# Performance work log

Hardware: AMD Instinct MI355X
Metric: run time of the kernel (lower is better)

Reference implementation:

```python
import jax, jax.numpy as jnp
import numpy as np
from jax import lax

EMB, HDIM, OBS_LEN = 64, 64, 8
BATCH, NSCENES, SCENE = 32768, 4096, 8
SEQ_LEN = 12


def setup_inputs() -> dict:
    key = jax.random.key(0)
    ks = jax.random.split(key, 16)
    obs_traj = jax.random.normal(ks[0], (OBS_LEN, BATCH, 2), jnp.float32)
    last_pos = jax.random.normal(ks[1], (BATCH, 2), jnp.float32)
    last_pos_rel = jax.random.normal(ks[2], (BATCH, 2), jnp.float32)
    starts = jnp.arange(NSCENES, dtype=jnp.int32) * SCENE
    seq_start_end = jnp.stack([starts, starts + SCENE], axis=1)  # (NSCENES, 2)
    # spatial_embedding: Linear(2, EMB)
    W_se = jax.random.normal(ks[3], (EMB, 2), jnp.float32) * 0.5
    b_se = jax.random.normal(ks[4], (EMB,), jnp.float32) * 0.1
    # weight-normed convs: w = g * v / ||v||_(in,k) per out-channel, bias init zero
    def conv_params(k, cout, cin, ksz):
        ka, kb = jax.random.split(k)
        std = np.sqrt(4.0 / (ksz * cin))
        v = jax.random.normal(ka, (cout, cin, ksz), jnp.float32) * std
        g = jax.random.uniform(kb, (cout,), jnp.float32, 0.5, 1.5)
        b = jnp.zeros((cout,), jnp.float32)
        return v, g, b
    v1, g1, b1 = conv_params(ks[5], HDIM, EMB, 3)
    v2, g2, b2 = conv_params(ks[6], HDIM // 2, HDIM, 3)
    v3, g3, b3 = conv_params(ks[7], HDIM // 2, HDIM // 2, 3)
    # hidden2pos: Linear(2*HDIM, 2)
    W_hp = jax.random.normal(ks[8], (2, 2 * HDIM), jnp.float32) * 0.05
    b_hp = jax.random.normal(ks[9], (2,), jnp.float32) * 0.05
    return {"obs_traj": obs_traj, "last_pos": last_pos, "last_pos_rel": last_pos_rel,
            "W_se": W_se, "b_se": b_se,
            "v1": v1, "g1": g1, "b1": b1,
            "v2": v2, "g2": g2, "b2": b2,
            "v3": v3, "g3": g3, "b3": b3,
            "W_hp": W_hp, "b_hp": b_hp,
            "seq_start_end": seq_start_end, "seq_len": SEQ_LEN}


def _wn_conv_relu(x, v, g, b):
    # weight-norm: w[o] = g[o] * v[o] / ||v[o]||  (norm over in-channels and kernel)
    norm = jnp.sqrt(jnp.sum(v * v, axis=(1, 2)))
    w = v * (g / norm)[:, None, None]
    y = lax.conv_general_dilated(x, w, (1,), 'VALID',
                                 dimension_numbers=('NCH', 'OIH', 'NCH'))
    return jax.nn.relu(y + b[None, :, None])


def reference(obs_traj, last_pos, last_pos_rel,
              W_se, b_se, v1, g1, b1, v2, g2, b2, v3, g3, b3, W_hp, b_hp,
              seq_start_end, seq_len):
    batch = last_pos.shape[0]
    nseg = seq_start_end.shape[0]
    h_dim = v1.shape[0]
    # scene id for each pedestrian (segments are contiguous [start,end) ranges)
    seg = jnp.searchsorted(seq_start_end[:, 0], jnp.arange(batch), side='right') - 1
    # obs_traj embedding -> (batch, EMB, OBS_LEN)
    emb = obs_traj @ W_se.T + b_se            # (T, B, EMB)
    obs_emb0 = jnp.transpose(emb, (1, 2, 0))  # (B, EMB, T)

    def step(carry, _):
        obs_emb, lp = carry
        s = _wn_conv_relu(obs_emb, v1, g1, b1)   # (B, H, T-2)
        s = _wn_conv_relu(s, v2, g2, b2)         # (B, H/2, T-4)
        s = _wn_conv_relu(s, v3, g3, b3)         # (B, H/2, T-6)
        s = s.reshape(batch, h_dim)              # (H/2)*(T-6) == H
        mx = jax.ops.segment_max(s, seg, num_segments=nseg)  # ragged per-scene max
        st = jnp.concatenate([s, mx[seg]], axis=1)           # (B, 2H)
        rel = st @ W_hp.T + b_hp                 # (B, 2)
        lp = rel + lp
        dec = rel @ W_se.T + b_se                # (B, EMB)
        obs_emb = jnp.concatenate([obs_emb[:, :, 1:], dec[:, :, None]], axis=2)
        return (obs_emb, lp), rel

    _, rels = lax.scan(step, (obs_emb0, last_pos), None, length=seq_len)
    return rels  # (seq_len, batch, 2)
```

## Files before the change

kernel.cpp:

```cpp
#include <hip/hip_runtime.h>

#define BATCH 32768
#define SEQLEN 12
#define NBLK 512

typedef short short8 __attribute__((ext_vector_type(8)));
typedef float f32x4 __attribute__((ext_vector_type(4)));
typedef unsigned short ushort_t;

static __device__ __forceinline__ unsigned short f2bf(float x) {
    unsigned u = __float_as_uint(x);
    return (unsigned short)((u + 0x7FFFu + ((u >> 16) & 1u)) >> 16);
}
static __device__ __forceinline__ float bf2f(unsigned short h) {
    return __uint_as_float(((unsigned)h) << 16);
}

#define MFMA __builtin_amdgcn_mfma_f32_16x16x32_bf16


#define C1PED(PX, PY, QX, QY, RX, RY, PPED) do {                              \
    float v_ = cK1;                                                           \
    v_ = fmaf(ccA0, PX, v_); v_ = fmaf(ccB0, PY, v_);                         \
    v_ = fmaf(ccA1, QX, v_); v_ = fmaf(ccB1, QY, v_);                         \
    v_ = fmaf(ccA2, RX, v_); v_ = fmaf(ccB2, RY, v_);                         \
    v_ = fmaxf(v_, 0.f);                                                      \
    ushort_t h_ = f2bf(v_);                                                   \
    s1sh[wv][PPED][lane] = h_;                                                \
    s1sl[wv][PPED][lane] = f2bf(v_ - bf2f(h_));                               \
} while(0)

#define S1_FRAGREAD(SL) do {                                                  \
    s1fh[SL][0] = *(const short8*)&s1sh[wv][n][kg*8];                         \
    s1fh[SL][1] = *(const short8*)&s1sh[wv][n][32 + kg*8];                    \
    s1fl[SL][0] = *(const short8*)&s1sl[wv][n][kg*8];                         \
    s1fl[SL][1] = *(const short8*)&s1sl[wv][n][32 + kg*8];                    \
} while(0)

#define CONV1COL(SA, SB, SC, SL) do {                                         \
    _Pragma("unroll")                                                         \
    for (int pp_ = 0; pp_ < 8; ++pp_) {                                       \
        float4 fa_ = *(const float4*)&pos_s[wv][SA][2*pp_][0];                \
        float4 fb_ = *(const float4*)&pos_s[wv][SB][2*pp_][0];                \
        float4 fc_ = *(const float4*)&pos_s[wv][SC][2*pp_][0];                \
        C1PED(fa_.x, fa_.y, fb_.x, fb_.y, fc_.x, fc_.y, 2*pp_);               \
        C1PED(fa_.z, fa_.w, fb_.z, fb_.w, fc_.z, fc_.w, 2*pp_+1);             \
    }                                                                         \
    S1_FRAGREAD(SL);                                                          \
} while(0)

#define CONV2COL(CM3) do {                                                    \
    _Pragma("unroll")                                                         \
    for (int T = 0; T < 2; ++T) {                                             \
        f32x4 a1 = {0.f,0.f,0.f,0.f}, a2 = {0.f,0.f,0.f,0.f},                 \
              a3 = {0.f,0.f,0.f,0.f};                                         \
        _Pragma("unroll")                                                     \
        for (int kb = 0; kb < 6; ++kb) {                                      \
            const int sl = ((CM3) + (kb >> 1)) % 3, ich = kb & 1;             \
            const short8 wh = *(const short8*)&c2wh[T*6+kb][lane][0];         \
            const short8 wl = *(const short8*)&c2wl[T*6+kb][lane][0];         \
            a1 = MFMA(wh, s1fh[sl][ich], a1, 0, 0, 0);                        \
            a2 = MFMA(wh, s1fl[sl][ich], a2, 0, 0, 0);                        \
            a3 = MFMA(wl, s1fh[sl][ich], a3, 0, 0, 0);                        \
        }                                                                     \
        const float4 bb = *(const float4*)&b2s[T*16 + kg*4];                  \
        float w0 = fmaxf(a1[0]+a2[0]+a3[0]+bb.x, 0.f);                        \
        float w1 = fmaxf(a1[1]+a2[1]+a3[1]+bb.y, 0.f);                        \
        float w2 = fmaxf(a1[2]+a2[2]+a3[2]+bb.z, 0.f);                        \
        float w3 = fmaxf(a1[3]+a2[3]+a3[3]+bb.w, 0.f);                        \
        ushort_t h0=f2bf(w0), h1=f2bf(w1), h2=f2bf(w2), h3=f2bf(w3);          \
        *(uint2*)&s2sh[wv][n][T*16 + kg*4] = make_uint2(                      \
            (unsigned)h0 | ((unsigned)h1 << 16),                              \
            (unsigned)h2 | ((unsigned)h3 << 16));                             \
        *(uint2*)&s2sl[wv][n][T*16 + kg*4] = make_uint2(                      \
            (unsigned)f2bf(w0-bf2f(h0)) | ((unsigned)f2bf(w1-bf2f(h1)) << 16),\
            (unsigned)f2bf(w2-bf2f(h2)) | ((unsigned)f2bf(w3-bf2f(h3)) << 16));\
    }                                                                         \
    s2fh[(CM3)] = *(const short8*)&s2sh[wv][n][kg*8];                         \
    s2fl[(CM3)] = *(const short8*)&s2sl[wv][n][kg*8];                         \
} while(0)

#define CONV3COL(VM3, PARI) do {                                              \
    _Pragma("unroll")                                                         \
    for (int T = 0; T < 2; ++T) {                                             \
        f32x4 a1 = {0.f,0.f,0.f,0.f}, a2 = {0.f,0.f,0.f,0.f},                 \
              a3 = {0.f,0.f,0.f,0.f};                                         \
        _Pragma("unroll")                                                     \
        for (int kb = 0; kb < 3; ++kb) {                                      \
            const int sl = ((VM3) + kb) % 3;                                  \
            const short8 wh = *(const short8*)&c3wh[T*3+kb][lane][0];         \
            a1 = MFMA(wh, s2fh[sl], a1, 0, 0, 0);                             \
            a2 = MFMA(wh, s2fl[sl], a2, 0, 0, 0);                             \
            a3 = MFMA(c3l[T][kb], s2fh[sl], a3, 0, 0, 0);                     \
        }                                                                     \
        const float4 b3v = *(const float4*)&b3s[T*16 + kg*4];                 \
        float m0 = fmaxf(a1[0]+a2[0]+a3[0]+b3v.x, 0.f);                       \
        float m1 = fmaxf(a1[1]+a2[1]+a3[1]+b3v.y, 0.f);                       \
        float m2 = fmaxf(a1[2]+a2[2]+a3[2]+b3v.z, 0.f);                       \
        float m3 = fmaxf(a1[3]+a2[3]+a3[3]+b3v.w, 0.f);                       \
        c3c[PARI][T] = (f32x4){m0, m1, m2, m3};                               \
        _Pragma("unroll")                                                     \
        for (int msk = 1; msk <= 4; msk <<= 1) {                              \
            m0 = fmaxf(m0, __shfl_xor(m0, msk));                              \
            m1 = fmaxf(m1, __shfl_xor(m1, msk));                              \
            m2 = fmaxf(m2, __shfl_xor(m2, msk));                              \
            m3 = fmaxf(m3, __shfl_xor(m3, msk));                              \
        }                                                                     \
        mxc[PARI][T] = (f32x4){m0, m1, m2, m3};                               \
    }                                                                         \
} while(0)

#define STAGE2(T0) do {                                                       \
    const int tau_ = (T0) + (lane >> 5);                                      \
    const int p_ = (lane >> 1) & 15, c_ = lane & 1;                           \
    pos_s[wv][tau_ & 3][p_][c_] =                                             \
        obs[(size_t)(tau_*BATCH + bped + p_)*2 + c_];                         \
} while(0)

#define STEP(K) do {                                                          \
    const int st = sbase + (K);                                               \
    float pv0a = 0.f, pv0b = 0.f, pv1a = 0.f, pv1b = 0.f;                     \
    {                                                                         \
        const float4* wq = (const float4*)&whp_s[kg][0];                      \
        _Pragma("unroll")                                                     \
        for (int q = 0; q < 16; ++q) {                                        \
            float4 ww = wq[q];                                                \
            _Pragma("unroll")                                                 \
            for (int e = 0; e < 4; ++e) {                                     \
                const int j2 = (q & 7)*4 + e;                                 \
                const int jj = j2 & 15;                                       \
                const int T = jj >> 3, r = (jj >> 1) & 3, col = jj & 1;       \
                const int par = col ? (((K)+1) & 1) : ((K) & 1);              \
                float val = (j2 < 16) ? c3c[par][T][r] : mxc[par][T][r];      \
                float wv_ = (e==0)?ww.x:(e==1)?ww.y:(e==2)?ww.z:ww.w;         \
                if (q < 8) { if (q & 1) pv0b = fmaf(wv_, val, pv0b);          \
                             else       pv0a = fmaf(wv_, val, pv0a); }        \
                else       { if (q & 1) pv1b = fmaf(wv_, val, pv1b);          \
                             else       pv1a = fmaf(wv_, val, pv1a); }        \
            }                                                                 \
        }                                                                     \
    }                                                                         \
    float pv0 = pv0a + pv0b, pv1 = pv1a + pv1b;                               \
    pv0 += __shfl_xor(pv0, 16); pv0 += __shfl_xor(pv0, 32);                   \
    pv1 += __shfl_xor(pv1, 16); pv1 += __shfl_xor(pv1, 32);                   \
    const float r0 = pv0 + bhp0, r1 = pv1 + bhp1;                             \
    if (lane < 16) {                                                          \
        float2 o; o.x = r0; o.y = r1;                                         \
        *(float2*)&out[(size_t)(st*BATCH + bped + lane)*2] = o;               \
    }                                                                         \
    if (st < SEQLEN-1) {                                                      \
        if (lane < 16) {                                                      \
            float2 o2; o2.x = r0; o2.y = r1;                                  \
            *(float2*)&pos_s[wv][st & 3][lane][0] = o2;         \
        }                                                                     \
        CONV1COL((st+2)&3, (st+3)&3, st&3, (K)%3);              \
        CONV2COL(((K)+1)%3);                                    \
        CONV3COL(((K)+2)%3, (K)&1);                             \
    }                                                                         \
} while(0)

__global__ __launch_bounds__(256, 2)
void enc_wp(const float* __restrict__ obs,
            const float* __restrict__ Wse, const float* __restrict__ bse,
            const float* __restrict__ v1, const float* __restrict__ g1, const float* __restrict__ b1,
            const float* __restrict__ v2, const float* __restrict__ g2, const float* __restrict__ b2,
            const float* __restrict__ v3, const float* __restrict__ g3, const float* __restrict__ b3,
            const float* __restrict__ Whp, const float* __restrict__ bhp,
            float* __restrict__ out)
{
    __shared__ __align__(16) ushort_t s1sh[4][16][72], s1sl[4][16][72];
    __shared__ __align__(16) ushort_t s2sh[4][16][40], s2sl[4][16][40];
    __shared__ __align__(16) float    pos_s[4][4][16][2];
    __shared__ __align__(16) float    whp_s[4][68];
    __shared__ __align__(16) ushort_t c2wh[12][64][8], c2wl[12][64][8];
    __shared__ __align__(16) ushort_t c3wh[6][64][8];
    __shared__ __align__(16) float    b2s[32], b3s[32];

    const int tid  = threadIdx.x;
    const int wv   = tid >> 6;
    const int lane = tid & 63;
    const int n    = lane & 15, kg = lane >> 4;
    const int bped = (blockIdx.x*4 + wv)*16;

    float* scr   = (float*)&s1sh[0][0][0];
    float* wse_s = scr;
    float* bse_s = scr + 128;
    float* sc2_s = scr + 192;
    float* sc3_s = scr + 224;

    if (wv == 0) {
        wse_s[lane] = Wse[lane]; wse_s[64 + lane] = Wse[64 + lane];
        bse_s[lane] = bse[lane];
        if (lane < 32) {
            b2s[lane] = b2[lane];
            const float* v = v2 + lane*192; float s = 0.f;
            for (int j = 0; j < 192; ++j) s += v[j]*v[j];
            sc2_s[lane] = g2[lane] / sqrtf(s);
        } else {
            b3s[lane-32] = b3[lane-32];
            const float* v = v3 + (lane-32)*96; float s = 0.f;
            for (int j = 0; j < 96; ++j) s += v[j]*v[j];
            sc3_s[lane-32] = g3[lane-32] / sqrtf(s);
        }
        #pragma unroll
        for (int q = 0; q < 4; ++q) {
            int d = lane >> 5, jp = lane & 31, jj = jp & 15;
            int T = jj >> 3, r = (jj >> 1) & 3, col = jj & 1;
            int off = (T*16 + q*4 + r)*2 + col + ((jp >= 16) ? 64 : 0);
            whp_s[q][lane] = Whp[d*128 + off];
        }
    }
    __syncthreads();

    if (wv == 0) {
        #pragma unroll
        for (int f = 0; f < 12; ++f) {
            const int T = f / 6, kb = f % 6;
            const int oc = T*16 + n, tap = kb >> 1, ich = kb & 1;
            const float s2s = sc2_s[oc];
            #pragma unroll
            for (int j = 0; j < 8; ++j) {
                const int ic = ich*32 + kg*8 + j;
                float w = v2[(size_t)(oc*64 + ic)*3 + tap] * s2s;
                ushort_t hb = f2bf(w);
                c2wh[f][lane][j] = hb;
                c2wl[f][lane][j] = f2bf(w - bf2f(hb));
            }
        }
    } else if (wv == 1) {
        #pragma unroll
        for (int f = 0; f < 6; ++f) {
            const int T = f / 3, kb = f % 3;
            const int oc = T*16 + n;
            const float s3s = sc3_s[oc];
            #pragma unroll
            for (int j = 0; j < 8; ++j) {
                const int ic = kg*8 + j;
                c3wh[f][lane][j] = f2bf(v3[(size_t)(oc*32 + ic)*3 + kb] * s3s);
            }
        }
    }

    float ccA0, ccA1, ccA2, ccB0, ccB1, ccB2, cK1;
    {
        const float* v = v1 + lane*192; float s = 0.f;
        for (int j = 0; j < 192; ++j) s += v[j]*v[j];
        const float sc1 = g1[lane] / sqrtf(s);
        float dA0=0,dA1=0,dA2=0,dB0=0,dB1=0,dB2=0,dC0=0,dC1=0,dC2=0;
        const float* vr = v1 + lane*192;
        #pragma unroll 4
        for (int ic = 0; ic < 64; ++ic) {
            float w0 = vr[ic*3], w1 = vr[ic*3+1], w2 = vr[ic*3+2];
            float we0 = wse_s[ic*2], we1 = wse_s[ic*2+1], be = bse_s[ic];
            dA0 = fmaf(w0, we0, dA0); dB0 = fmaf(w0, we1, dB0); dC0 = fmaf(w0, be, dC0);
            dA1 = fmaf(w1, we0, dA1); dB1 = fmaf(w1, we1, dB1); dC1 = fmaf(w1, be, dC1);
            dA2 = fmaf(w2, we0, dA2); dB2 = fmaf(w2, we1, dB2); dC2 = fmaf(w2, be, dC2);
        }
        ccA0 = sc1*dA0; ccA1 = sc1*dA1; ccA2 = sc1*dA2;
        ccB0 = sc1*dB0; ccB1 = sc1*dB1; ccB2 = sc1*dB2;
        cK1  = fmaf(sc1, (dC0 + dC1) + dC2, b1[lane]);
    }
    short8 c3l[2][3];
    #pragma unroll
    for (int T = 0; T < 2; ++T) {
        const int oc = T*16 + n;
        const float s3s = sc3_s[oc];
        #pragma unroll
        for (int kb = 0; kb < 3; ++kb) {
            #pragma unroll
            for (int j = 0; j < 8; ++j) {
                const int ic = kg*8 + j;
                float w = v3[(size_t)(oc*32 + ic)*3 + kb] * s3s;
                c3l[T][kb][j] = (short)f2bf(w - bf2f(f2bf(w)));
            }
        }
    }
    const float bhp0 = bhp[0], bhp1 = bhp[1];
    __syncthreads();

    short8 s1fh[3][2], s1fl[3][2], s2fh[3], s2fl[3];
    f32x4 c3c[2][2], mxc[2][2];

    STAGE2(0); STAGE2(2);
    CONV1COL(0, 1, 2, 0);
    CONV1COL(1, 2, 3, 1);
    STAGE2(4);
    CONV1COL(2, 3, 0, 2);
    CONV2COL(0);
    CONV1COL(3, 0, 1, 0);
    CONV2COL(1);
    STAGE2(6);
    CONV1COL(0, 1, 2, 1);
    CONV2COL(2);
    CONV3COL(0, 0);
    CONV1COL(1, 2, 3, 2);
    CONV2COL(0);
    CONV3COL(1, 1);

    #pragma unroll 1
    for (int hh = 0; hh < 2; ++hh) {
        const int sbase = hh * 6;
        STEP(0); STEP(1); STEP(2); STEP(3); STEP(4); STEP(5);
    }
}

extern "C" void kernel_launch(void* const* d_in, const int* in_sizes, int n_in,
                              void* d_out, int out_size, void* d_ws, size_t ws_size,
                              hipStream_t stream)
{
    const float* obs = (const float*)d_in[0];
    const float* Wse = (const float*)d_in[3];
    const float* bse = (const float*)d_in[4];
    const float* v1  = (const float*)d_in[5];
    const float* g1  = (const float*)d_in[6];
    const float* b1  = (const float*)d_in[7];
    const float* v2  = (const float*)d_in[8];
    const float* g2  = (const float*)d_in[9];
    const float* b2  = (const float*)d_in[10];
    const float* v3  = (const float*)d_in[11];
    const float* g3  = (const float*)d_in[12];
    const float* b3  = (const float*)d_in[13];
    const float* Whp = (const float*)d_in[14];
    const float* bhp = (const float*)d_in[15];

    enc_wp<<<NBLK, 256, 0, stream>>>(obs, Wse, bse, v1, g1, b1, v2, g2, b2,
                                     v3, g3, b3, Whp, bhp, (float*)d_out);
}
```

Before: 175.2 us.

## Compute conv1 directly in MFMA fragment layout, drop LDS staging, use DPP reductions

```diff
diff --git a/kernel.cpp b/kernel.cpp
--- a/kernel.cpp
+++ b/kernel.cpp
@@ -18,35 +18,41 @@
 
 #define MFMA __builtin_amdgcn_mfma_f32_16x16x32_bf16
 
-
-#define C1PED(PX, PY, QX, QY, RX, RY, PPED) do {                              \
-    float v_ = cK1;                                                           \
-    v_ = fmaf(ccA0, PX, v_); v_ = fmaf(ccB0, PY, v_);                         \
-    v_ = fmaf(ccA1, QX, v_); v_ = fmaf(ccB1, QY, v_);                         \
-    v_ = fmaf(ccA2, RX, v_); v_ = fmaf(ccB2, RY, v_);                         \
-    v_ = fmaxf(v_, 0.f);                                                      \
-    ushort_t h_ = f2bf(v_);                                                   \
-    s1sh[wv][PPED][lane] = h_;                                                \
-    s1sl[wv][PPED][lane] = f2bf(v_ - bf2f(h_));                               \
-} while(0)
-
-#define S1_FRAGREAD(SL) do {                                                  \
-    s1fh[SL][0] = *(const short8*)&s1sh[wv][n][kg*8];                         \
-    s1fh[SL][1] = *(const short8*)&s1sh[wv][n][32 + kg*8];                    \
-    s1fl[SL][0] = *(const short8*)&s1sl[wv][n][kg*8];                         \
-    s1fl[SL][1] = *(const short8*)&s1sl[wv][n][32 + kg*8];                    \
-} while(0)
-
-#define CONV1COL(SA, SB, SC, SL) do {                                         \
+#define FMAXDPP(X, CTRL) \
+    fmaxf((X), __int_as_float(__builtin_amdgcn_mov_dpp(__float_as_int(X), (CTRL), 0xF, 0xF, true)))
+
+
+#define CONV1D(SA_, SB_, R0_, R1_, SL_) do {                                  \
+    float2 pa_ = *(const float2*)&pos_s[wv][SA_][n][0];                       \
+    float2 pb_ = *(const float2*)&pos_s[wv][SB_][n][0];                       \
     _Pragma("unroll")                                                         \
-    for (int pp_ = 0; pp_ < 8; ++pp_) {                                       \
-        float4 fa_ = *(const float4*)&pos_s[wv][SA][2*pp_][0];                \
-        float4 fb_ = *(const float4*)&pos_s[wv][SB][2*pp_][0];                \
-        float4 fc_ = *(const float4*)&pos_s[wv][SC][2*pp_][0];                \
-        C1PED(fa_.x, fa_.y, fb_.x, fb_.y, fc_.x, fc_.y, 2*pp_);               \
-        C1PED(fa_.z, fa_.w, fb_.z, fb_.w, fc_.z, fc_.w, 2*pp_+1);             \
-    }                                                                         \
-    S1_FRAGREAD(SL);                                                          \
+    for (int ich_ = 0; ich_ < 2; ++ich_) {                                    \
+        const int cb_ = ich_*32 + kg*8;                                       \
+        float cf_[7][8];                                                      \
+        _Pragma("unroll")                                                     \
+        for (int k_ = 0; k_ < 7; ++k_) {                                      \
+            *(float4*)&cf_[k_][0] = *(const float4*)&c1t[k_][cb_];            \
+            *(float4*)&cf_[k_][4] = *(const float4*)&c1t[k_][cb_ + 4];        \
+        }                                                                     \
+        short8 sh_, sl_;                                                      \
+        _Pragma("unroll")                                                     \
+        for (int j_ = 0; j_ < 8; ++j_) {                                      \
+            float v_ = cf_[6][j_];                                            \
+            v_ = fmaf(cf_[0][j_], pa_.x, v_); v_ = fmaf(cf_[1][j_], pa_.y, v_);\
+            v_ = fmaf(cf_[2][j_], pb_.x, v_); v_ = fmaf(cf_[3][j_], pb_.y, v_);\
+            v_ = fmaf(cf_[4][j_], (R0_), v_); v_ = fmaf(cf_[5][j_], (R1_), v_);\
+            v_ = fmaxf(v_, 0.f);                                              \
+            ushort_t h_ = f2bf(v_);                                           \
+            sh_[j_] = (short)h_;                                              \
+            sl_[j_] = (short)f2bf(v_ - bf2f(h_));                             \
+        }                                                                     \
+        s1fh[SL_][ich_] = sh_; s1fl[SL_][ich_] = sl_;                         \
+    }                                                                         \
+} while(0)
+
+#define WCONV1D(SA_, SB_, SC_, SL_) do {                                      \
+    float2 pc_ = *(const float2*)&pos_s[wv][SC_][n][0];                       \
+    CONV1D(SA_, SB_, pc_.x, pc_.y, SL_);                                      \
 } while(0)
 
 #define CONV2COL(CM3) do {                                                    \
@@ -99,13 +105,14 @@
         float m2 = fmaxf(a1[2]+a2[2]+a3[2]+b3v.z, 0.f);                       \
         float m3 = fmaxf(a1[3]+a2[3]+a3[3]+b3v.w, 0.f);                       \
         c3c[PARI][T] = (f32x4){m0, m1, m2, m3};                               \
-        _Pragma("unroll")                                                     \
-        for (int msk = 1; msk <= 4; msk <<= 1) {                              \
-            m0 = fmaxf(m0, __shfl_xor(m0, msk));                              \
-            m1 = fmaxf(m1, __shfl_xor(m1, msk));                              \
-            m2 = fmaxf(m2, __shfl_xor(m2, msk));                              \
-            m3 = fmaxf(m3, __shfl_xor(m3, msk));                              \
-        }                                                                     \
+        m0 = FMAXDPP(m0, 0xB1); m0 = FMAXDPP(m0, 0x4E);                       \
+        m0 = fmaxf(m0, __shfl_xor(m0, 4));                                    \
+        m1 = FMAXDPP(m1, 0xB1); m1 = FMAXDPP(m1, 0x4E);                       \
+        m1 = fmaxf(m1, __shfl_xor(m1, 4));                                    \
+        m2 = FMAXDPP(m2, 0xB1); m2 = FMAXDPP(m2, 0x4E);                       \
+        m2 = fmaxf(m2, __shfl_xor(m2, 4));                                    \
+        m3 = FMAXDPP(m3, 0xB1); m3 = FMAXDPP(m3, 0x4E);                       \
+        m3 = fmaxf(m3, __shfl_xor(m3, 4));                                    \
         mxc[PARI][T] = (f32x4){m0, m1, m2, m3};                               \
     }                                                                         \
 } while(0)
@@ -120,24 +127,21 @@
 #define STEP(K) do {                                                          \
     const int st = sbase + (K);                                               \
     float pv0a = 0.f, pv0b = 0.f, pv1a = 0.f, pv1b = 0.f;                     \
-    {                                                                         \
-        const float4* wq = (const float4*)&whp_s[kg][0];                      \
-        _Pragma("unroll")                                                     \
-        for (int q = 0; q < 16; ++q) {                                        \
-            float4 ww = wq[q];                                                \
-            _Pragma("unroll")                                                 \
-            for (int e = 0; e < 4; ++e) {                                     \
-                const int j2 = (q & 7)*4 + e;                                 \
-                const int jj = j2 & 15;                                       \
-                const int T = jj >> 3, r = (jj >> 1) & 3, col = jj & 1;       \
-                const int par = col ? (((K)+1) & 1) : ((K) & 1);              \
-                float val = (j2 < 16) ? c3c[par][T][r] : mxc[par][T][r];      \
-                float wv_ = (e==0)?ww.x:(e==1)?ww.y:(e==2)?ww.z:ww.w;         \
-                if (q < 8) { if (q & 1) pv0b = fmaf(wv_, val, pv0b);          \
-                             else       pv0a = fmaf(wv_, val, pv0a); }        \
-                else       { if (q & 1) pv1b = fmaf(wv_, val, pv1b);          \
-                             else       pv1a = fmaf(wv_, val, pv1a); }        \
-            }                                                                 \
+    _Pragma("unroll")                                                         \
+    for (int q = 0; q < 16; ++q) {                                            \
+        float4 ww = w4[q];                                                    \
+        _Pragma("unroll")                                                     \
+        for (int e = 0; e < 4; ++e) {                                         \
+            const int j2 = (q & 7)*4 + e;                                     \
+            const int jj = j2 & 15;                                           \
+            const int T = jj >> 3, r = (jj >> 1) & 3, col = jj & 1;           \
+            const int par = col ? (((K)+1) & 1) : ((K) & 1);                  \
+            float val = (j2 < 16) ? c3c[par][T][r] : mxc[par][T][r];          \
+            float wv_ = (e==0)?ww.x:(e==1)?ww.y:(e==2)?ww.z:ww.w;             \
+            if (q < 8) { if (q & 1) pv0b = fmaf(wv_, val, pv0b);              \
+                         else       pv0a = fmaf(wv_, val, pv0a); }            \
+            else       { if (q & 1) pv1b = fmaf(wv_, val, pv1b);              \
+                         else       pv1a = fmaf(wv_, val, pv1a); }            \
         }                                                                     \
     }                                                                         \
     float pv0 = pv0a + pv0b, pv1 = pv1a + pv1b;                               \
@@ -153,7 +157,7 @@
             float2 o2; o2.x = r0; o2.y = r1;                                  \
             *(float2*)&pos_s[wv][st & 3][lane][0] = o2;         \
         }                                                                     \
-        CONV1COL((st+2)&3, (st+3)&3, st&3, (K)%3);              \
+        CONV1D((st+2)&3, (st+3)&3, r0, r1, (K)%3);              \
         CONV2COL(((K)+1)%3);                                    \
         CONV3COL(((K)+2)%3, (K)&1);                             \
     }                                                                         \
@@ -168,13 +172,13 @@
             const float* __restrict__ Whp, const float* __restrict__ bhp,
             float* __restrict__ out)
 {
-    __shared__ __align__(16) ushort_t s1sh[4][16][72], s1sl[4][16][72];
     __shared__ __align__(16) ushort_t s2sh[4][16][40], s2sl[4][16][40];
     __shared__ __align__(16) float    pos_s[4][4][16][2];
     __shared__ __align__(16) float    whp_s[4][68];
     __shared__ __align__(16) ushort_t c2wh[12][64][8], c2wl[12][64][8];
     __shared__ __align__(16) ushort_t c3wh[6][64][8];
     __shared__ __align__(16) float    b2s[32], b3s[32];
+    __shared__ __align__(16) float    c1t[7][64];
 
     const int tid  = threadIdx.x;
     const int wv   = tid >> 6;
@@ -182,7 +186,7 @@
     const int n    = lane & 15, kg = lane >> 4;
     const int bped = (blockIdx.x*4 + wv)*16;
 
-    float* scr   = (float*)&s1sh[0][0][0];
+    float* scr   = (float*)&s2sh[0][0][0];
     float* wse_s = scr;
     float* bse_s = scr + 128;
     float* sc2_s = scr + 192;
@@ -213,6 +217,24 @@
     __syncthreads();
 
     if (wv == 0) {
+        const float* v = v1 + lane*192; float s = 0.f;
+        for (int j = 0; j < 192; ++j) s += v[j]*v[j];
+        const float sc1 = g1[lane] / sqrtf(s);
+        float dA0=0,dA1=0,dA2=0,dB0=0,dB1=0,dB2=0,dC0=0,dC1=0,dC2=0;
+        const float* vr = v1 + lane*192;
+        #pragma unroll 4
+        for (int ic = 0; ic < 64; ++ic) {
+            float w0 = vr[ic*3], w1 = vr[ic*3+1], w2 = vr[ic*3+2];
+            float we0 = wse_s[ic*2], we1 = wse_s[ic*2+1], be = bse_s[ic];
+            dA0 = fmaf(w0, we0, dA0); dB0 = fmaf(w0, we1, dB0); dC0 = fmaf(w0, be, dC0);
+            dA1 = fmaf(w1, we0, dA1); dB1 = fmaf(w1, we1, dB1); dC1 = fmaf(w1, be, dC1);
+            dA2 = fmaf(w2, we0, dA2); dB2 = fmaf(w2, we1, dB2); dC2 = fmaf(w2, be, dC2);
+        }
+        c1t[0][lane] = sc1*dA0; c1t[1][lane] = sc1*dB0;
+        c1t[2][lane] = sc1*dA1; c1t[3][lane] = sc1*dB1;
+        c1t[4][lane] = sc1*dA2; c1t[5][lane] = sc1*dB2;
+        c1t[6][lane] = fmaf(sc1, (dC0 + dC1) + dC2, b1[lane]);
+    } else if (wv == 2) {
         #pragma unroll
         for (int f = 0; f < 12; ++f) {
             const int T = f / 6, kb = f % 6;
@@ -239,26 +261,6 @@
                 c3wh[f][lane][j] = f2bf(v3[(size_t)(oc*32 + ic)*3 + kb] * s3s);
             }
         }
-    }
-
-    float ccA0, ccA1, ccA2, ccB0, ccB1, ccB2, cK1;
-    {
-        const float* v = v1 + lane*192; float s = 0.f;
-        for (int j = 0; j < 192; ++j) s += v[j]*v[j];
-        const float sc1 = g1[lane] / sqrtf(s);
-        float dA0=0,dA1=0,dA2=0,dB0=0,dB1=0,dB2=0,dC0=0,dC1=0,dC2=0;
-        const float* vr = v1 + lane*192;
-        #pragma unroll 4
-        for (int ic = 0; ic < 64; ++ic) {
-            float w0 = vr[ic*3], w1 = vr[ic*3+1], w2 = vr[ic*3+2];
-            float we0 = wse_s[ic*2], we1 = wse_s[ic*2+1], be = bse_s[ic];
-            dA0 = fmaf(w0, we0, dA0); dB0 = fmaf(w0, we1, dB0); dC0 = fmaf(w0, be, dC0);
-            dA1 = fmaf(w1, we0, dA1); dB1 = fmaf(w1, we1, dB1); dC1 = fmaf(w1, be, dC1);
-            dA2 = fmaf(w2, we0, dA2); dB2 = fmaf(w2, we1, dB2); dC2 = fmaf(w2, be, dC2);
-        }
-        ccA0 = sc1*dA0; ccA1 = sc1*dA1; ccA2 = sc1*dA2;
-        ccB0 = sc1*dB0; ccB1 = sc1*dB1; ccB2 = sc1*dB2;
-        cK1  = fmaf(sc1, (dC0 + dC1) + dC2, b1[lane]);
     }
     short8 c3l[2][3];
     #pragma unroll
@@ -275,6 +277,9 @@
             }
         }
     }
+    float4 w4[16];
+    #pragma unroll
+    for (int q = 0; q < 16; ++q) w4[q] = *(const float4*)&whp_s[kg][q*4];
     const float bhp0 = bhp[0], bhp1 = bhp[1];
     __syncthreads();
 
@@ -282,18 +287,18 @@
     f32x4 c3c[2][2], mxc[2][2];
 
     STAGE2(0); STAGE2(2);
-    CONV1COL(0, 1, 2, 0);
-    CONV1COL(1, 2, 3, 1);
+    WCONV1D(0, 1, 2, 0);
+    WCONV1D(1, 2, 3, 1);
     STAGE2(4);
-    CONV1COL(2, 3, 0, 2);
+    WCONV1D(2, 3, 0, 2);
     CONV2COL(0);
-    CONV1COL(3, 0, 1, 0);
+    WCONV1D(3, 0, 1, 0);
     CONV2COL(1);
     STAGE2(6);
-    CONV1COL(0, 1, 2, 1);
+    WCONV1D(0, 1, 2, 1);
     CONV2COL(2);
     CONV3COL(0, 0);
-    CONV1COL(1, 2, 3, 2);
+    WCONV1D(1, 2, 3, 2);
     CONV2COL(0);
     CONV3COL(1, 1);
 
```

After: 363.2 us. 2.07x slower.
